# Optimization experiments

Hardware: AMD Instinct MI355X
Metric: run time of the kernel (lower is better)

Reference implementation:

```python
import jax, jax.numpy as jnp
import numpy as np

N = 100000
E = 1600000
D = 128
EPS = 1e-5


def setup_inputs() -> dict:
    key = jax.random.key(0)
    ks = jax.random.split(key, 8)
    s = 1.0 / np.sqrt(D)
    feats = jax.random.normal(ks[0], (N, D), dtype=jnp.float32)
    src = jax.random.randint(ks[1], (E,), 0, N, dtype=jnp.int32)
    dst = jax.random.randint(ks[2], (E,), 0, N, dtype=jnp.int32)
    W_gcn = jax.random.normal(ks[3], (D, D), dtype=jnp.float32) * s
    b_gcn = jnp.zeros((D,), dtype=jnp.float32)
    W_res = jax.random.normal(ks[4], (D, D), dtype=jnp.float32) * s
    b_res = jnp.zeros((D,), dtype=jnp.float32)
    g1 = jnp.ones((D,), dtype=jnp.float32)
    be1 = jnp.zeros((D,), dtype=jnp.float32)
    g2 = jnp.ones((D,), dtype=jnp.float32)
    be2 = jnp.zeros((D,), dtype=jnp.float32)
    return {"feats": feats, "W_gcn": W_gcn, "b_gcn": b_gcn, "W_res": W_res,
            "b_res": b_res, "g1": g1, "be1": be1, "g2": g2, "be2": be2,
            "src": src, "dst": dst}


def _batchnorm(x, gamma, beta):
    # BatchNorm1d, training mode: biased batch stats over the node dim
    mu = jnp.mean(x, axis=0)
    var = jnp.var(x, axis=0)
    return gamma * (x - mu) * jax.lax.rsqrt(var + EPS) + beta


def reference(feats, W_gcn, b_gcn, W_res, b_res, g1, be1, g2, be2, src, dst):
    n = feats.shape[0]
    # GraphConv(norm='none'): sum-aggregate neighbor feats then linear (in<=out)
    agg = jax.ops.segment_sum(feats[src], dst, num_segments=n)  # [N, D]
    h = jax.nn.relu(agg @ W_gcn + b_gcn)
    # dgllife GCNLayer internal residual: activation(Linear(feats))
    res = jax.nn.relu(feats @ W_res + b_res)
    h = _batchnorm(h + res, g1, be1)
    # outer ResidualGCNLayer: Identity residual (in_feats==out_feats) + BN
    out = _batchnorm(h + feats, g2, be2)
    return out
```

## Files before the change

kernel.cpp:

```cpp
#include <hip/hip_runtime.h>
#include <hip/hip_bf16.h>
#include <stdint.h>

#define NN 100000
#define EE 1600000
#define DD 128
#define EPSV 1e-5f
#define WWIN 128
#define NB 782
#define NCLS 8
#define NSEG (NB * NCLS)
#define ITEMS (EE / 4)
#define ITEMS_PER_CLS (ITEMS / NCLS)
#define SORTCAP 4096

typedef __attribute__((ext_vector_type(8))) short short8;
typedef __attribute__((ext_vector_type(4))) float floatx4;
typedef unsigned short u16;

union S8 { short8 v; short s[8]; unsigned short u[8]; };

__device__ __forceinline__ float bf2f(u16 u) {
    return __uint_as_float(((unsigned int)u) << 16);
}
__device__ __forceinline__ u16 f2bf(float f) {
    unsigned int x = __float_as_uint(f);
    x += 0x7FFFu + ((x >> 16) & 1u);
    return (u16)(x >> 16);
}


__global__ __launch_bounds__(256) void k_convert(
    const float* __restrict__ ff,
    const float* __restrict__ Wg, const float* __restrict__ Wr,
    const float* __restrict__ bg, const float* __restrict__ br,
    const float* __restrict__ g1, const float* __restrict__ g2,
    const float* __restrict__ be2,
    u16* __restrict__ fc, u16* __restrict__ pc,
    int* __restrict__ flag, int* __restrict__ done,
    int* __restrict__ cnt, float* __restrict__ stats)
{
    const int bx = blockIdx.x;
    const int tx = threadIdx.x;
    if (bx < 27) {
        const int idx = bx * 256 + tx;
        if (idx < 5 * DD) stats[idx] = 0.f;
        else {
            const int j = idx - 5 * DD;
            if (j < NSEG) cnt[j] = 0;
            else if (j == NSEG) *done = 0;
        }
        return;
    }
    __shared__ int dc;
    if (tx == 0) dc = 0;
    __syncthreads();
    const float dv = fabsf(ff[tx]);
    if (dv > 1e-3f && dv < 1e3f) atomicAdd(&dc, 1);
    __syncthreads();
    const int myflag = (dc >= 128) ? 1 : 0;
    if (bx == 27 && tx == 0) *flag = myflag;
    if (!myflag) return;

    if (bx < 158) {
        const int i = (bx - 27) * 256 + tx;
        if (i >= 33408) return;
        float v;
        if (i < 16384)      v = Wg[i];
        else if (i < 32768) v = Wr[i - 16384];
        else {
            const int j = i - 32768;
            const int a = j >> 7, o = j & 127;
            v = (a == 0) ? bg[o] : (a == 1) ? br[o] : (a == 2) ? g1[o]
              : (a == 3) ? g2[o] : be2[o];
        }
        pc[i] = f2bf(v);
        return;
    }
    const int bid = bx - 158;
    const size_t P = (size_t)NN * (DD / 4);
    for (size_t i = (size_t)bid * 256 + tx; i < P; i += (size_t)1024 * 256) {
        const float4 v = *(const float4*)(ff + 4 * i);
        uint2 o;
        o.x = (unsigned int)f2bf(v.x) | ((unsigned int)f2bf(v.y) << 16);
        o.y = (unsigned int)f2bf(v.z) | ((unsigned int)f2bf(v.w) << 16);
        *(uint2*)(fc + 4 * i) = o;
    }
}

__global__ __launch_bounds__(256) void k_hist2(
    const int* __restrict__ dst, int* __restrict__ cnt,
    int* __restrict__ done, int* __restrict__ off, int* __restrict__ cursor)
{
    __shared__ int lc[NB];
    const int tx   = threadIdx.x;
    const int cls  = blockIdx.x & 7;
    const int blk  = blockIdx.x >> 3;
    const int nblk = gridDim.x >> 3;
    const int it0  = cls * ITEMS_PER_CLS;
    const int it1  = it0 + ITEMS_PER_CLS;
    for (int i = tx; i < NB; i += 256) lc[i] = 0;
    __syncthreads();
    const int4* __restrict__ dst4 = (const int4*)dst;
    for (int it = it0 + blk * 256 + tx; it < it1; it += nblk * 256) {
        const int4 d = dst4[it];
        atomicAdd(&lc[d.x >> 7], 1);
        atomicAdd(&lc[d.y >> 7], 1);
        atomicAdd(&lc[d.z >> 7], 1);
        atomicAdd(&lc[d.w >> 7], 1);
    }
    __syncthreads();
    for (int i = tx; i < NB; i += 256) {
        const int v = lc[i];
        if (v) atomicAdd(&cnt[i * NCLS + cls], v);
    }
    __threadfence();
    __shared__ int last;
    if (tx == 0) last = (atomicAdd(done, 1) == (int)gridDim.x - 1) ? 1 : 0;
    __syncthreads();
    if (!last) return;

    const int lane = tx & 63, w = tx >> 6;
    __shared__ int wsum[4];
    __shared__ int carry;
    if (tx == 0) carry = 0;
    __syncthreads();
    for (int base = 0; base < NSEG; base += 256) {
        const int i = base + tx;
        int v = 0;
        if (i < NSEG)
            v = __hip_atomic_load(&cnt[i], __ATOMIC_RELAXED, __HIP_MEMORY_SCOPE_AGENT);
        int incl = v;
#pragma unroll
        for (int d = 1; d < 64; d <<= 1) {
            const int n = __shfl_up(incl, d, 64);
            if (lane >= d) incl += n;
        }
        if (lane == 63) wsum[w] = incl;
        __syncthreads();
        if (tx == 0) {
            int s = 0;
#pragma unroll
            for (int k = 0; k < 4; ++k) { s += wsum[k]; wsum[k] = s; }
        }
        __syncthreads();
        const int c = carry;
        const int woff = (w == 0) ? 0 : wsum[w - 1];
        if (i < NSEG) {
            const int excl = c + woff + incl - v;
            off[i] = excl;
            cursor[i] = excl;
        }
        __syncthreads();
        if (tx == 0) carry = c + wsum[3];
        __syncthreads();
    }
    if (tx == 0) off[NSEG] = carry;
}

__global__ __launch_bounds__(256) void k_bin(
    const int* __restrict__ src, const int* __restrict__ dst,
    int* __restrict__ cursor, unsigned int* __restrict__ arena)
{
    __shared__ int lc[NB], lb[NB];
    const int cls  = blockIdx.x & 7;
    const int blk  = blockIdx.x >> 3;
    const int nblk = gridDim.x >> 3;
    const int it0  = cls * ITEMS_PER_CLS;
    const int it1  = it0 + ITEMS_PER_CLS;
    const int4* __restrict__ dst4 = (const int4*)dst;
    const int4* __restrict__ src4 = (const int4*)src;
    for (int i = threadIdx.x; i < NB; i += 256) lc[i] = 0;
    __syncthreads();
    for (int it = it0 + blk * blockDim.x + threadIdx.x; it < it1;
         it += nblk * blockDim.x) {
        const int4 d = dst4[it];
        atomicAdd(&lc[d.x >> 7], 1);
        atomicAdd(&lc[d.y >> 7], 1);
        atomicAdd(&lc[d.z >> 7], 1);
        atomicAdd(&lc[d.w >> 7], 1);
    }
    __syncthreads();
    for (int i = threadIdx.x; i < NB; i += 256) {
        const int v = lc[i];
        lb[i] = v ? atomicAdd(&cursor[i * NCLS + cls], v) : 0;
    }
    __syncthreads();
    for (int i = threadIdx.x; i < NB; i += 256) lc[i] = 0;
    __syncthreads();
    for (int it = it0 + blk * blockDim.x + threadIdx.x; it < it1;
         it += nblk * blockDim.x) {
        const int4 d = dst4[it];
        const int4 s = src4[it];
        int wv, p;
        wv = d.x >> 7; p = lb[wv] + atomicAdd(&lc[wv], 1);
        arena[p] = ((unsigned int)(d.x & 127) << 17) | (unsigned int)s.x;
        wv = d.y >> 7; p = lb[wv] + atomicAdd(&lc[wv], 1);
        arena[p] = ((unsigned int)(d.y & 127) << 17) | (unsigned int)s.y;
        wv = d.z >> 7; p = lb[wv] + atomicAdd(&lc[wv], 1);
        arena[p] = ((unsigned int)(d.z & 127) << 17) | (unsigned int)s.z;
        wv = d.w >> 7; p = lb[wv] + atomicAdd(&lc[wv], 1);
        arena[p] = ((unsigned int)(d.w & 127) << 17) | (unsigned int)s.w;
    }
}

__global__ __launch_bounds__(256) void k_sortgather(
    const int* __restrict__ flag,
    const u16* __restrict__ feats_raw, const u16* __restrict__ feats_c,
    const unsigned int* __restrict__ arena, const int* __restrict__ off,
    u16* __restrict__ aggb)
{
    __shared__ unsigned int buf[SORTCAP];
    __shared__ int sorted[SORTCAP];
    __shared__ int cnt_[WWIN], pref[WWIN], cur[WWIN];
    const u16* __restrict__ F = (*flag != 0) ? feats_c : feats_raw;
    const int tx = threadIdx.x;
    const int b  = blockIdx.x;
    const int s0 = off[b * NCLS];
    int len = off[b * NCLS + NCLS] - s0;
    if (len > SORTCAP) len = SORTCAP;
    if (tx < WWIN) cnt_[tx] = 0;
    __syncthreads();
    for (int i = tx; i < len; i += 256) {
        const unsigned int p = arena[s0 + i];
        buf[i] = p;
        atomicAdd(&cnt_[p >> 17], 1);
    }
    __syncthreads();
    if (tx < WWIN) pref[tx] = cnt_[tx];
    __syncthreads();
    for (int d = 1; d < WWIN; d <<= 1) {
        int v = 0;
        if (tx < WWIN && tx >= d) v = pref[tx - d];
        __syncthreads();
        if (tx < WWIN) pref[tx] += v;
        __syncthreads();
    }
    if (tx < WWIN) cur[tx] = pref[tx] - cnt_[tx];
    __syncthreads();
    for (int i = tx; i < len; i += 256) {
        const unsigned int p = buf[i];
        const int pos = atomicAdd(&cur[p >> 17], 1);
        sorted[pos] = (int)(p & 0x1FFFFu);
    }
    __syncthreads();

    const int lane = tx & 63;
    const int l16  = lane & 15;
    const int wv   = tx >> 6;
    for (int it = 0; it < 8; ++it) {
        const int nloc = wv * 32 + it * 4 + (lane >> 4);
        const int node = b * WWIN + nloc;
        const int deg  = cnt_[nloc];
        const int rs   = pref[nloc] - deg;
        float a0 = 0.f, a1 = 0.f, a2 = 0.f, a3 = 0.f;
        float a4 = 0.f, a5 = 0.f, a6 = 0.f, a7 = 0.f;
        int j = 0;
        for (; j + 8 <= deg; j += 8) {
            uint4 vv[8];
#pragma unroll
            for (int q = 0; q < 8; ++q) {
                const int s = sorted[rs + j + q];
                vv[q] = *(const uint4*)(F + (size_t)s * DD + l16 * 8);
            }
#pragma unroll
            for (int q = 0; q < 8; ++q) {
                a0 += bf2f((u16)(vv[q].x & 0xFFFFu));
                a1 += bf2f((u16)(vv[q].x >> 16));
                a2 += bf2f((u16)(vv[q].y & 0xFFFFu));
                a3 += bf2f((u16)(vv[q].y >> 16));
                a4 += bf2f((u16)(vv[q].z & 0xFFFFu));
                a5 += bf2f((u16)(vv[q].z >> 16));
                a6 += bf2f((u16)(vv[q].w & 0xFFFFu));
                a7 += bf2f((u16)(vv[q].w >> 16));
            }
        }
        for (; j < deg; ++j) {
            const int s = sorted[rs + j];
            const uint4 v = *(const uint4*)(F + (size_t)s * DD + l16 * 8);
            a0 += bf2f((u16)(v.x & 0xFFFFu));
            a1 += bf2f((u16)(v.x >> 16));
            a2 += bf2f((u16)(v.y & 0xFFFFu));
            a3 += bf2f((u16)(v.y >> 16));
            a4 += bf2f((u16)(v.z & 0xFFFFu));
            a5 += bf2f((u16)(v.z >> 16));
            a6 += bf2f((u16)(v.w & 0xFFFFu));
            a7 += bf2f((u16)(v.w >> 16));
        }
        if (node < NN) {
            uint4 o;
            o.x = (unsigned int)f2bf(a0) | ((unsigned int)f2bf(a1) << 16);
            o.y = (unsigned int)f2bf(a2) | ((unsigned int)f2bf(a3) << 16);
            o.z = (unsigned int)f2bf(a4) | ((unsigned int)f2bf(a5) << 16);
            o.w = (unsigned int)f2bf(a6) | ((unsigned int)f2bf(a7) << 16);
            *(uint4*)(aggb + (size_t)node * DD + l16 * 8) = o;
        }
    }
}

__global__ __launch_bounds__(256) void k_gemm(
    const int* __restrict__ flag,
    const u16* __restrict__ aggb,
    const u16* __restrict__ feats_raw, const u16* __restrict__ feats_c,
    const u16* __restrict__ Wg_raw, const u16* __restrict__ bg_raw,
    const u16* __restrict__ Wr_raw, const u16* __restrict__ br_raw,
    const u16* __restrict__ pc,
    u16* __restrict__ t_out, float* __restrict__ stats)
{
    const bool f32 = (*flag != 0);
    const u16* __restrict__ F  = f32 ? feats_c     : feats_raw;
    const u16* __restrict__ Wg = f32 ? pc          : Wg_raw;
    const u16* __restrict__ Wr = f32 ? pc + 16384  : Wr_raw;
    const u16* __restrict__ bg = f32 ? pc + 32768  : bg_raw;
    const u16* __restrict__ br = f32 ? pc + 32896  : br_raw;

    const int lane = threadIdx.x & 63;
    const int wv   = threadIdx.x >> 6;
    const int l15  = lane & 15;
    const int quad = lane >> 4;
    const int c0 = wv * 16 + l15;
    const int c1 = 64 + wv * 16 + l15;

    S8 fg0[4], fg1[4], fr0[4], fr1[4];
#pragma unroll
    for (int kb = 0; kb < 4; ++kb) {
        const int kr = kb * 32 + quad * 8;
#pragma unroll
        for (int j = 0; j < 8; ++j) {
            fg0[kb].u[j] = Wg[(size_t)(kr + j) * DD + c0];
            fg1[kb].u[j] = Wg[(size_t)(kr + j) * DD + c1];
            fr0[kb].u[j] = Wr[(size_t)(kr + j) * DD + c0];
            fr1[kb].u[j] = Wr[(size_t)(kr + j) * DD + c1];
        }
    }
    const float bgc0 = bf2f(bg[c0]), bgc1 = bf2f(bg[c1]);
    const float brc0 = bf2f(br[c0]), brc1 = bf2f(br[c1]);

    float s_t0 = 0.f, s_t1 = 0.f, s_tt0 = 0.f, s_tt1 = 0.f;
    float s_f0 = 0.f, s_f1 = 0.f, s_ff0 = 0.f, s_ff1 = 0.f;
    float s_tf0 = 0.f, s_tf1 = 0.f;

    for (int tile = blockIdx.x; tile < NN / 16; tile += gridDim.x) {
        const int row0 = tile * 16;
        const int arow = row0 + l15;
        floatx4 ag0 = {0.f,0.f,0.f,0.f}, ag1 = {0.f,0.f,0.f,0.f};
        floatx4 ar0 = {0.f,0.f,0.f,0.f}, ar1 = {0.f,0.f,0.f,0.f};
#pragma unroll
        for (int kb = 0; kb < 4; ++kb) {
            const int kbase = kb * 32 + quad * 8;
            S8 av, ff;
            av.v = *(const short8*)(aggb + (size_t)arow * DD + kbase);
            ff.v = *(const short8*)(F    + (size_t)arow * DD + kbase);
            ag0 = __builtin_amdgcn_mfma_f32_16x16x32_bf16(av.v, fg0[kb].v, ag0, 0, 0, 0);
            ag1 = __builtin_amdgcn_mfma_f32_16x16x32_bf16(av.v, fg1[kb].v, ag1, 0, 0, 0);
            ar0 = __builtin_amdgcn_mfma_f32_16x16x32_bf16(ff.v, fr0[kb].v, ar0, 0, 0, 0);
            ar1 = __builtin_amdgcn_mfma_f32_16x16x32_bf16(ff.v, fr1[kb].v, ar1, 0, 0, 0);
        }
#pragma unroll
        for (int r = 0; r < 4; ++r) {
            const int row = row0 + quad * 4 + r;
            const u16 tb0 = f2bf(fmaxf(ag0[r] + bgc0, 0.f) + fmaxf(ar0[r] + brc0, 0.f));
            const u16 tb1 = f2bf(fmaxf(ag1[r] + bgc1, 0.f) + fmaxf(ar1[r] + brc1, 0.f));
            t_out[(size_t)row * DD + c0] = tb0;
            t_out[(size_t)row * DD + c1] = tb1;
            const float t0 = bf2f(tb0), t1 = bf2f(tb1);
            const float fv0 = bf2f(F[(size_t)row * DD + c0]);
            const float fv1 = bf2f(F[(size_t)row * DD + c1]);
            s_t0  += t0;        s_t1  += t1;
            s_tt0 += t0 * t0;   s_tt1 += t1 * t1;
            s_f0  += fv0;       s_f1  += fv1;
            s_ff0 += fv0 * fv0; s_ff1 += fv1 * fv1;
            s_tf0 += t0 * fv0;  s_tf1 += t1 * fv1;
        }
    }

#define QRED(x) x += __shfl_xor(x, 16, 64); x += __shfl_xor(x, 32, 64);
    QRED(s_t0)  QRED(s_t1)  QRED(s_tt0) QRED(s_tt1)
    QRED(s_f0)  QRED(s_f1)  QRED(s_ff0) QRED(s_ff1)
    QRED(s_tf0) QRED(s_tf1)
#undef QRED
    if (quad == 0) {
        unsafeAtomicAdd(&stats[0 * DD + c0], s_t0);
        unsafeAtomicAdd(&stats[0 * DD + c1], s_t1);
        unsafeAtomicAdd(&stats[1 * DD + c0], s_tt0);
        unsafeAtomicAdd(&stats[1 * DD + c1], s_tt1);
        unsafeAtomicAdd(&stats[2 * DD + c0], s_f0);
        unsafeAtomicAdd(&stats[2 * DD + c1], s_f1);
        unsafeAtomicAdd(&stats[3 * DD + c0], s_ff0);
        unsafeAtomicAdd(&stats[3 * DD + c1], s_ff1);
        unsafeAtomicAdd(&stats[4 * DD + c0], s_tf0);
        unsafeAtomicAdd(&stats[4 * DD + c1], s_tf1);
    }
}

__global__ __launch_bounds__(256) void k_final(
    const int* __restrict__ flag,
    const u16* __restrict__ t,
    const u16* __restrict__ feats_raw, const u16* __restrict__ feats_c,
    const u16* __restrict__ g1_raw, const u16* __restrict__ g2_raw,
    const u16* __restrict__ be2_raw, const u16* __restrict__ pc,
    const float* __restrict__ stats,
    void* __restrict__ out)
{
    const bool f32 = (*flag != 0);
    const u16* __restrict__ F   = f32 ? feats_c    : feats_raw;
    const u16* __restrict__ g1  = f32 ? pc + 33024 : g1_raw;
    const u16* __restrict__ g2  = f32 ? pc + 33152 : g2_raw;
    const u16* __restrict__ be2 = f32 ? pc + 33280 : be2_raw;

    __shared__ float sA[DD], sB[DD], sG[DD];
    if (threadIdx.x < DD) {
        const int c = threadIdx.x;
        const float invN = 1.0f / (float)NN;
        const float St  = stats[c],          Stt = stats[DD + c];
        const float Sf  = stats[2 * DD + c], Sff = stats[3 * DD + c];
        const float Stf = stats[4 * DD + c];
        const float mu1  = St * invN;
        const float vart = fmaxf(Stt * invN - mu1 * mu1, 0.f);
        const float muf  = Sf * invN;
        const float varf = fmaxf(Sff * invN - muf * muf, 0.f);
        const float cov  = Stf * invN - mu1 * muf;
        const float r1   = rsqrtf(vart + EPSV);
        const float a1   = bf2f(g1[c]) * r1;
        const float var2 = fmaxf(a1 * a1 * vart + 2.f * a1 * cov + varf, 0.f);
        const float r2   = rsqrtf(var2 + EPSV);
        const float g2r2 = bf2f(g2[c]) * r2;
        sA[c] = g2r2 * a1;
        sB[c] = g2r2;
        sG[c] = bf2f(be2[c]) - g2r2 * (a1 * mu1 + muf);
    }
    __syncthreads();

    float* outf = (float*)out;
    u16*   outb = (u16*)out;
    const size_t P = (size_t)NN * (DD / 4);
    for (size_t i = (size_t)blockIdx.x * blockDim.x + threadIdx.x; i < P;
         i += (size_t)gridDim.x * blockDim.x) {
        const int c = ((int)(i & 31)) * 4;
        const uint2 tv = *(const uint2*)(t + 4 * i);
        const uint2 fv = *(const uint2*)(F + 4 * i);
        const float o0 = sA[c]     * bf2f((u16)(tv.x & 0xFFFFu))
                       + sB[c]     * bf2f((u16)(fv.x & 0xFFFFu)) + sG[c];
        const float o1 = sA[c + 1] * bf2f((u16)(tv.x >> 16))
                       + sB[c + 1] * bf2f((u16)(fv.x >> 16)) + sG[c + 1];
        const float o2 = sA[c + 2] * bf2f((u16)(tv.y & 0xFFFFu))
                       + sB[c + 2] * bf2f((u16)(fv.y & 0xFFFFu)) + sG[c + 2];
        const float o3 = sA[c + 3] * bf2f((u16)(tv.y >> 16))
                       + sB[c + 3] * bf2f((u16)(fv.y >> 16)) + sG[c + 3];
        if (f32) {
            float4 o; o.x = o0; o.y = o1; o.z = o2; o.w = o3;
            *(float4*)(outf + 4 * i) = o;
        } else {
            uint2 ov;
            ov.x = (unsigned int)f2bf(o0) | ((unsigned int)f2bf(o1) << 16);
            ov.y = (unsigned int)f2bf(o2) | ((unsigned int)f2bf(o3) << 16);
            *(uint2*)(outb + 4 * i) = ov;
        }
    }
}

extern "C" void kernel_launch(void* const* d_in, const int* in_sizes, int n_in,
                              void* d_out, int out_size, void* d_ws, size_t ws_size,
                              hipStream_t stream) {
    const u16* feats = (const u16*)d_in[0];
    const u16* Wg    = (const u16*)d_in[1];
    const u16* bg    = (const u16*)d_in[2];
    const u16* Wr    = (const u16*)d_in[3];
    const u16* br    = (const u16*)d_in[4];
    const u16* g1    = (const u16*)d_in[5];
    const u16* g2    = (const u16*)d_in[7];
    const u16* be2   = (const u16*)d_in[8];
    const int* src = (const int*)d_in[9];
    const int* dst = (const int*)d_in[10];

    char* ws = (char*)d_ws;
    u16*          aggb    = (u16*)  ws;
    u16*          t       = (u16*)  (ws + 25600000);
    u16*          feats_c = (u16*)  (ws + 51200000);
    u16*          pc      = (u16*)  (ws + 76800000);
    float*        stats   = (float*)(ws + 76866816);
    int*          flag    = (int*)  (ws + 76869376);
    int*          done    = (int*)  (ws + 76869380);
    int*          cnt     = (int*)  (ws + 76869632);
    int*          off     = (int*)  (ws + 76894656);
    int*          cursor  = (int*)  (ws + 76919684);
    unsigned int* arena   = (unsigned int*)(ws + 77344712);

    k_convert<<<1182, 256, 0, stream>>>((const float*)d_in[0],
        (const float*)d_in[1], (const float*)d_in[3], (const float*)d_in[2],
        (const float*)d_in[4], (const float*)d_in[5], (const float*)d_in[7],
        (const float*)d_in[8], feats_c, pc, flag, done, cnt, stats);

    k_hist2<<<256, 256, 0, stream>>>(dst, cnt, done, off, cursor);
    k_bin  <<<256, 256, 0, stream>>>(src, dst, cursor, arena);
    k_sortgather<<<NB, 256, 0, stream>>>(flag, feats, feats_c, arena, off, aggb);
    k_gemm <<<1024, 256, 0, stream>>>(flag, aggb, feats, feats_c, Wg, bg, Wr, br, pc, t, stats);
    k_final<<<2048, 256, 0, stream>>>(flag, t, feats, feats_c, g1, g2, be2, pc, stats, d_out);
}
```

Baseline: 313.8 us.

## Replace histogram-scan binning with fixed-capacity windows and deterministic stat reduction

Removes the separate histogram and prefix-scan kernel. Each destination window now gets a fixed-capacity slot (WCAP) in the arena, and a single binning kernel appends into it through per-window padded cursors. The GEMM grid shrinks to 128 blocks and writes per-block partial statistics, which a small kernel then reduces instead of using global float atomics. The arena reuses the t buffer region. The risk is silent truncation if a window receives more edges than WCAP, and the smaller GEMM grid may cut parallelism.

```diff
diff --git a/kernel.cpp b/kernel.cpp
--- a/kernel.cpp
+++ b/kernel.cpp
@@ -8,11 +8,13 @@
 #define EPSV 1e-5f
 #define WWIN 128
 #define NB 782
-#define NCLS 8
-#define NSEG (NB * NCLS)
+#define WCAP 2304
 #define ITEMS (EE / 4)
-#define ITEMS_PER_CLS (ITEMS / NCLS)
-#define SORTCAP 4096
+#define BINB 128
+#define ITEMS_PER_BIN (ITEMS / BINB)
+#define SORTCAP 2304
+#define NSTAT 640
+#define GEMMB 128
 
 typedef __attribute__((ext_vector_type(8))) short short8;
 typedef __attribute__((ext_vector_type(4))) float floatx4;
@@ -37,19 +39,12 @@
     const float* __restrict__ g1, const float* __restrict__ g2,
     const float* __restrict__ be2,
     u16* __restrict__ fc, u16* __restrict__ pc,
-    int* __restrict__ flag, int* __restrict__ done,
-    int* __restrict__ cnt, float* __restrict__ stats)
+    int* __restrict__ flag, int* __restrict__ cursor)
 {
     const int bx = blockIdx.x;
     const int tx = threadIdx.x;
-    if (bx < 27) {
-        const int idx = bx * 256 + tx;
-        if (idx < 5 * DD) stats[idx] = 0.f;
-        else {
-            const int j = idx - 5 * DD;
-            if (j < NSEG) cnt[j] = 0;
-            else if (j == NSEG) *done = 0;
-        }
+    if (bx == 0) {
+        for (int w = tx; w < NB; w += 256) cursor[w * 16] = 0;
         return;
     }
     __shared__ int dc;
@@ -59,11 +54,11 @@
     if (dv > 1e-3f && dv < 1e3f) atomicAdd(&dc, 1);
     __syncthreads();
     const int myflag = (dc >= 128) ? 1 : 0;
-    if (bx == 27 && tx == 0) *flag = myflag;
+    if (bx == 1 && tx == 0) *flag = myflag;
     if (!myflag) return;
 
-    if (bx < 158) {
-        const int i = (bx - 27) * 256 + tx;
+    if (bx < 132) {
+        const int i = (bx - 1) * 256 + tx;
         if (i >= 33408) return;
         float v;
         if (i < 16384)      v = Wg[i];
@@ -77,7 +72,7 @@
         pc[i] = f2bf(v);
         return;
     }
-    const int bid = bx - 158;
+    const int bid = bx - 132;
     const size_t P = (size_t)NN * (DD / 4);
     for (size_t i = (size_t)bid * 256 + tx; i < P; i += (size_t)1024 * 256) {
         const float4 v = *(const float4*)(ff + 4 * i);
@@ -88,21 +83,19 @@
     }
 }
 
-__global__ __launch_bounds__(256) void k_hist2(
-    const int* __restrict__ dst, int* __restrict__ cnt,
-    int* __restrict__ done, int* __restrict__ off, int* __restrict__ cursor)
-{
-    __shared__ int lc[NB];
-    const int tx   = threadIdx.x;
-    const int cls  = blockIdx.x & 7;
-    const int blk  = blockIdx.x >> 3;
-    const int nblk = gridDim.x >> 3;
-    const int it0  = cls * ITEMS_PER_CLS;
-    const int it1  = it0 + ITEMS_PER_CLS;
-    for (int i = tx; i < NB; i += 256) lc[i] = 0;
-    __syncthreads();
+__global__ __launch_bounds__(256) void k_bin2(
+    const int* __restrict__ src, const int* __restrict__ dst,
+    int* __restrict__ cursor, unsigned int* __restrict__ arena)
+{
+    __shared__ int lc[NB], lb[NB];
+    const int bx  = blockIdx.x;
+    const int it0 = bx * ITEMS_PER_BIN;
+    const int it1 = it0 + ITEMS_PER_BIN;
     const int4* __restrict__ dst4 = (const int4*)dst;
-    for (int it = it0 + blk * 256 + tx; it < it1; it += nblk * 256) {
+    const int4* __restrict__ src4 = (const int4*)src;
+    for (int i = threadIdx.x; i < NB; i += 256) lc[i] = 0;
+    __syncthreads();
+    for (int it = it0 + threadIdx.x; it < it1; it += 256) {
         const int4 d = dst4[it];
         atomicAdd(&lc[d.x >> 7], 1);
         atomicAdd(&lc[d.y >> 7], 1);
@@ -110,86 +103,14 @@
         atomicAdd(&lc[d.w >> 7], 1);
     }
     __syncthreads();
-    for (int i = tx; i < NB; i += 256) {
-        const int v = lc[i];
-        if (v) atomicAdd(&cnt[i * NCLS + cls], v);
-    }
-    __threadfence();
-    __shared__ int last;
-    if (tx == 0) last = (atomicAdd(done, 1) == (int)gridDim.x - 1) ? 1 : 0;
-    __syncthreads();
-    if (!last) return;
-
-    const int lane = tx & 63, w = tx >> 6;
-    __shared__ int wsum[4];
-    __shared__ int carry;
-    if (tx == 0) carry = 0;
-    __syncthreads();
-    for (int base = 0; base < NSEG; base += 256) {
-        const int i = base + tx;
-        int v = 0;
-        if (i < NSEG)
-            v = __hip_atomic_load(&cnt[i], __ATOMIC_RELAXED, __HIP_MEMORY_SCOPE_AGENT);
-        int incl = v;
-#pragma unroll
-        for (int d = 1; d < 64; d <<= 1) {
-            const int n = __shfl_up(incl, d, 64);
-            if (lane >= d) incl += n;
-        }
-        if (lane == 63) wsum[w] = incl;
-        __syncthreads();
-        if (tx == 0) {
-            int s = 0;
-#pragma unroll
-            for (int k = 0; k < 4; ++k) { s += wsum[k]; wsum[k] = s; }
-        }
-        __syncthreads();
-        const int c = carry;
-        const int woff = (w == 0) ? 0 : wsum[w - 1];
-        if (i < NSEG) {
-            const int excl = c + woff + incl - v;
-            off[i] = excl;
-            cursor[i] = excl;
-        }
-        __syncthreads();
-        if (tx == 0) carry = c + wsum[3];
-        __syncthreads();
-    }
-    if (tx == 0) off[NSEG] = carry;
-}
-
-__global__ __launch_bounds__(256) void k_bin(
-    const int* __restrict__ src, const int* __restrict__ dst,
-    int* __restrict__ cursor, unsigned int* __restrict__ arena)
-{
-    __shared__ int lc[NB], lb[NB];
-    const int cls  = blockIdx.x & 7;
-    const int blk  = blockIdx.x >> 3;
-    const int nblk = gridDim.x >> 3;
-    const int it0  = cls * ITEMS_PER_CLS;
-    const int it1  = it0 + ITEMS_PER_CLS;
-    const int4* __restrict__ dst4 = (const int4*)dst;
-    const int4* __restrict__ src4 = (const int4*)src;
+    for (int w = threadIdx.x; w < NB; w += 256) {
+        const int v = lc[w];
+        lb[w] = v ? (w * WCAP + atomicAdd(&cursor[w * 16], v)) : 0;
+    }
+    __syncthreads();
     for (int i = threadIdx.x; i < NB; i += 256) lc[i] = 0;
     __syncthreads();
-    for (int it = it0 + blk * blockDim.x + threadIdx.x; it < it1;
-         it += nblk * blockDim.x) {
-        const int4 d = dst4[it];
-        atomicAdd(&lc[d.x >> 7], 1);
-        atomicAdd(&lc[d.y >> 7], 1);
-        atomicAdd(&lc[d.z >> 7], 1);
-        atomicAdd(&lc[d.w >> 7], 1);
-    }
-    __syncthreads();
-    for (int i = threadIdx.x; i < NB; i += 256) {
-        const int v = lc[i];
-        lb[i] = v ? atomicAdd(&cursor[i * NCLS + cls], v) : 0;
-    }
-    __syncthreads();
-    for (int i = threadIdx.x; i < NB; i += 256) lc[i] = 0;
-    __syncthreads();
-    for (int it = it0 + blk * blockDim.x + threadIdx.x; it < it1;
-         it += nblk * blockDim.x) {
+    for (int it = it0 + threadIdx.x; it < it1; it += 256) {
         const int4 d = dst4[it];
         const int4 s = src4[it];
         int wv, p;
@@ -207,7 +128,7 @@
 __global__ __launch_bounds__(256) void k_sortgather(
     const int* __restrict__ flag,
     const u16* __restrict__ feats_raw, const u16* __restrict__ feats_c,
-    const unsigned int* __restrict__ arena, const int* __restrict__ off,
+    const unsigned int* __restrict__ arena, const int* __restrict__ cursor,
     u16* __restrict__ aggb)
 {
     __shared__ unsigned int buf[SORTCAP];
@@ -216,9 +137,9 @@
     const u16* __restrict__ F = (*flag != 0) ? feats_c : feats_raw;
     const int tx = threadIdx.x;
     const int b  = blockIdx.x;
-    const int s0 = off[b * NCLS];
-    int len = off[b * NCLS + NCLS] - s0;
-    if (len > SORTCAP) len = SORTCAP;
+    const int s0 = b * WCAP;
+    int len = cursor[b * 16];
+    if (len > WCAP) len = WCAP;
     if (tx < WWIN) cnt_[tx] = 0;
     __syncthreads();
     for (int i = tx; i < len; i += 256) {
@@ -305,7 +226,7 @@
     const u16* __restrict__ Wg_raw, const u16* __restrict__ bg_raw,
     const u16* __restrict__ Wr_raw, const u16* __restrict__ br_raw,
     const u16* __restrict__ pc,
-    u16* __restrict__ t_out, float* __restrict__ stats)
+    u16* __restrict__ t_out, float* __restrict__ stats_part)
 {
     const bool f32 = (*flag != 0);
     const u16* __restrict__ F  = f32 ? feats_c     : feats_raw;
@@ -380,17 +301,28 @@
     QRED(s_tf0) QRED(s_tf1)
 #undef QRED
     if (quad == 0) {
-        unsafeAtomicAdd(&stats[0 * DD + c0], s_t0);
-        unsafeAtomicAdd(&stats[0 * DD + c1], s_t1);
-        unsafeAtomicAdd(&stats[1 * DD + c0], s_tt0);
-        unsafeAtomicAdd(&stats[1 * DD + c1], s_tt1);
-        unsafeAtomicAdd(&stats[2 * DD + c0], s_f0);
-        unsafeAtomicAdd(&stats[2 * DD + c1], s_f1);
-        unsafeAtomicAdd(&stats[3 * DD + c0], s_ff0);
-        unsafeAtomicAdd(&stats[3 * DD + c1], s_ff1);
-        unsafeAtomicAdd(&stats[4 * DD + c0], s_tf0);
-        unsafeAtomicAdd(&stats[4 * DD + c1], s_tf1);
-    }
+        float* sp = stats_part + (size_t)blockIdx.x * NSTAT;
+        sp[0 * DD + c0] = s_t0;   sp[0 * DD + c1] = s_t1;
+        sp[1 * DD + c0] = s_tt0;  sp[1 * DD + c1] = s_tt1;
+        sp[2 * DD + c0] = s_f0;   sp[2 * DD + c1] = s_f1;
+        sp[3 * DD + c0] = s_ff0;  sp[3 * DD + c1] = s_ff1;
+        sp[4 * DD + c0] = s_tf0;  sp[4 * DD + c1] = s_tf1;
+    }
+}
+
+__global__ __launch_bounds__(256) void k_statred(
+    const float* __restrict__ stats_part, float* __restrict__ stats)
+{
+    const int e = blockIdx.x * 256 + threadIdx.x;
+    if (e >= NSTAT) return;
+    float a0 = 0.f, a1 = 0.f, a2 = 0.f, a3 = 0.f;
+    for (int s = 0; s < GEMMB; s += 4) {
+        a0 += stats_part[(size_t)(s + 0) * NSTAT + e];
+        a1 += stats_part[(size_t)(s + 1) * NSTAT + e];
+        a2 += stats_part[(size_t)(s + 2) * NSTAT + e];
+        a3 += stats_part[(size_t)(s + 3) * NSTAT + e];
+    }
+    stats[e] = (a0 + a1) + (a2 + a3);
 }
 
 __global__ __launch_bounds__(256) void k_final(
@@ -474,26 +406,24 @@
     const int* dst = (const int*)d_in[10];
 
     char* ws = (char*)d_ws;
-    u16*          aggb    = (u16*)  ws;
-    u16*          t       = (u16*)  (ws + 25600000);
-    u16*          feats_c = (u16*)  (ws + 51200000);
-    u16*          pc      = (u16*)  (ws + 76800000);
-    float*        stats   = (float*)(ws + 76866816);
-    int*          flag    = (int*)  (ws + 76869376);
-    int*          done    = (int*)  (ws + 76869380);
-    int*          cnt     = (int*)  (ws + 76869632);
-    int*          off     = (int*)  (ws + 76894656);
-    int*          cursor  = (int*)  (ws + 76919684);
-    unsigned int* arena   = (unsigned int*)(ws + 77344712);
-
-    k_convert<<<1182, 256, 0, stream>>>((const float*)d_in[0],
+    u16*          aggb       = (u16*)ws;
+    u16*          t          = (u16*)(ws + 25600000);
+    unsigned int* arena      = (unsigned int*)(ws + 25600000);
+    u16*          feats_c    = (u16*)  (ws + 51200000);
+    u16*          pc         = (u16*)  (ws + 76800000);
+    float*        stats      = (float*)(ws + 76866816);
+    int*          flag       = (int*)  (ws + 76869376);
+    int*          cursor     = (int*)  (ws + 76869632);
+    float*        stats_part = (float*)(ws + 76944768);
+
+    k_convert<<<1156, 256, 0, stream>>>((const float*)d_in[0],
         (const float*)d_in[1], (const float*)d_in[3], (const float*)d_in[2],
         (const float*)d_in[4], (const float*)d_in[5], (const float*)d_in[7],
-        (const float*)d_in[8], feats_c, pc, flag, done, cnt, stats);
-
-    k_hist2<<<256, 256, 0, stream>>>(dst, cnt, done, off, cursor);
-    k_bin  <<<256, 256, 0, stream>>>(src, dst, cursor, arena);
-    k_sortgather<<<NB, 256, 0, stream>>>(flag, feats, feats_c, arena, off, aggb);
-    k_gemm <<<1024, 256, 0, stream>>>(flag, aggb, feats, feats_c, Wg, bg, Wr, br, pc, t, stats);
-    k_final<<<2048, 256, 0, stream>>>(flag, t, feats, feats_c, g1, g2, be2, pc, stats, d_out);
-}
+        (const float*)d_in[8], feats_c, pc, flag, cursor);
+
+    k_bin2      <<<BINB, 256, 0, stream>>>(src, dst, cursor, arena);
+    k_sortgather<<<NB, 256, 0, stream>>>(flag, feats, feats_c, arena, cursor, aggb);
+    k_gemm      <<<GEMMB, 256, 0, stream>>>(flag, aggb, feats, feats_c, Wg, bg, Wr, br, pc, t, stats_part);
+    k_statred   <<<3, 256, 0, stream>>>(stats_part, stats);
+    k_final     <<<2048, 256, 0, stream>>>(flag, t, feats, feats_c, g1, g2, be2, pc, stats, d_out);
+}
```

Measured after the change: 315.1 us. No clear change (+0.4%).
